# Kernel tuning notes

Hardware: AMD Instinct MI355X
Metric: run time of the kernel (lower is better)

The kernel has to match this reference:

```python
import jax, jax.numpy as jnp
import numpy as np

N, E = 20000, 320000
D_IN, HID, HEADS, OUT = 256, 64, 8, 64
K1 = int(np.ceil(0.75 * N))   # 15000 nodes after pool1
K2 = int(np.ceil(0.75 * K1))  # 11250 nodes after pool2
NEG = -1e30


def setup_inputs():
    key = jax.random.key(0)
    ks = jax.random.split(key, 24)
    s = 0.1
    rn = lambda k, shape: jax.random.normal(k, shape, jnp.float32) * s
    HH = HEADS * HID  # 512
    p = {}
    p["x"] = jax.random.normal(ks[0], (N, D_IN), jnp.float32)
    p["edge_index"] = jax.random.randint(ks[1], (2, E), 0, N, dtype=jnp.int32)
    # gat1: GATv2Conv(D_IN -> HID, heads=HEADS), concat output dim HH
    p["g1_wl"] = rn(ks[2], (D_IN, HH)); p["g1_wr"] = rn(ks[3], (D_IN, HH))
    p["g1_att"] = rn(ks[4], (HEADS, HID)); p["g1_b"] = jnp.zeros((HH,), jnp.float32)
    # pool1 scoring GNN: GATConv(HH -> 1, heads=1) + SelectTopK weight
    p["p1_w"] = rn(ks[5], (HH, 1)); p["p1_asrc"] = rn(ks[6], (1,)); p["p1_adst"] = rn(ks[7], (1,))
    p["p1_b"] = jnp.zeros((1,), jnp.float32); p["p1_sel"] = rn(ks[8], (1,)) + 0.5
    # gat2: GATv2Conv(HH -> HID, heads=1)
    p["g2_wl"] = rn(ks[9], (HH, HID)); p["g2_wr"] = rn(ks[10], (HH, HID))
    p["g2_att"] = rn(ks[11], (1, HID)); p["g2_b"] = jnp.zeros((HID,), jnp.float32)
    # pool2 scoring GNN: GATConv(HID -> 1)
    p["p2_w"] = rn(ks[12], (HID, 1)); p["p2_asrc"] = rn(ks[13], (1,)); p["p2_adst"] = rn(ks[14], (1,))
    p["p2_b"] = jnp.zeros((1,), jnp.float32); p["p2_sel"] = rn(ks[15], (1,)) + 0.5
    # MLP head
    p["l1_w"] = rn(ks[16], (2 * HH, HH)); p["l1_b"] = jnp.zeros((HH,), jnp.float32)
    d2 = OUT * (HEADS // 2); d3 = OUT * (HEADS // 4)
    p["l2_w"] = rn(ks[17], (HH, d2)); p["l2_b"] = jnp.zeros((d2,), jnp.float32)
    p["l3_w"] = rn(ks[18], (d2, d3)); p["l3_b"] = jnp.zeros((d3,), jnp.float32)
    p["l4_w"] = rn(ks[19], (d3, 2)); p["l4_b"] = jnp.zeros((2,), jnp.float32)
    return p


def _seg_softmax(e, dst, valid, n):
    # numerically stable segment softmax over destination nodes; invalid edges -> 0
    e = jnp.where(valid[:, None], e, NEG)
    m = jax.ops.segment_max(e, dst, num_segments=n)
    ex = jnp.exp(e - m[dst])
    ex = jnp.where(valid[:, None], ex, 0.0)
    den = jax.ops.segment_sum(ex, dst, num_segments=n)
    return ex / den[dst]


def gatv2(x, src, dst, valid, wl, wr, att, b):
    # GATv2Conv: score = att . LeakyReLU(Wl x_src + Wr x_dst), segment softmax, concat heads
    n = x.shape[0]
    h, c = att.shape
    xl = (x @ wl).reshape(n, h, c)
    xr = (x @ wr).reshape(n, h, c)
    loop = jnp.arange(n, dtype=src.dtype)  # add_self_loops=True
    s = jnp.concatenate([src, loop]); d = jnp.concatenate([dst, loop])
    v = jnp.concatenate([valid, jnp.ones((n,), bool)])
    m = jax.nn.leaky_relu(xl[s] + xr[d], 0.2)          # [E', H, C]
    e = jnp.einsum("ehc,hc->eh", m, att)               # [E', H]
    a = _seg_softmax(e, d, v, n)
    out = jax.ops.segment_sum(a[..., None] * xl[s], d, num_segments=n)
    return out.reshape(n, h * c) + b


def gat_score(x, src, dst, valid, w, asrc, adst, b):
    # GATConv(in -> 1, heads=1): per-node scalar projection score
    n = x.shape[0]
    xl = x @ w                                          # [n, 1]
    al = (xl * asrc).sum(-1); ar = (xl * adst).sum(-1)  # [n]
    loop = jnp.arange(n, dtype=src.dtype)
    s = jnp.concatenate([src, loop]); d = jnp.concatenate([dst, loop])
    v = jnp.concatenate([valid, jnp.ones((n,), bool)])
    e = jax.nn.leaky_relu(al[s] + ar[d], 0.2)[:, None]
    a = _seg_softmax(e, d, v, n)
    return jax.ops.segment_sum(a * xl[s], d, num_segments=n) + b


def sag_pool(x, src, dst, valid, k, w, asrc, adst, b, sel_w):
    # SAGPooling: GNN score -> tanh -> top-k -> x[perm]*score, edge filtering via mask
    attn = gat_score(x, src, dst, valid, w, asrc, adst, b)           # [n, 1]
    score = jnp.tanh((attn * sel_w).sum(-1) / jnp.linalg.norm(sel_w))  # SelectTopK
    vals, perm = jax.lax.top_k(score, k)
    xp = x[perm] * vals[:, None]
    new_id = jnp.full((x.shape[0],), -1, src.dtype).at[perm].set(jnp.arange(k, dtype=src.dtype))
    s2, d2 = new_id[src], new_id[dst]
    v2 = valid & (s2 >= 0) & (d2 >= 0)
    return xp, jnp.where(v2, s2, 0), jnp.where(v2, d2, 0), v2


def _forward(x, edge_index, g1_wl, g1_wr, g1_att, g1_b, p1_w, p1_asrc, p1_adst, p1_b, p1_sel,
             g2_wl, g2_wr, g2_att, g2_b, p2_w, p2_asrc, p2_adst, p2_b, p2_sel,
             l1_w, l1_b, l2_w, l2_b, l3_w, l3_b, l4_w, l4_b):
    src, dst = edge_index[0], edge_index[1]
    valid = jnp.ones((src.shape[0],), bool)
    h = jax.nn.relu(gatv2(x, src, dst, valid, g1_wl, g1_wr, g1_att, g1_b))
    h, s1, d1, v1 = sag_pool(h, src, dst, valid, K1, p1_w, p1_asrc, p1_adst, p1_b, p1_sel)
    # single graph -> global pools are plain reductions over nodes
    x1 = jnp.concatenate([h.max(0, keepdims=True), h.mean(0, keepdims=True)], axis=1)
    h2 = jax.nn.relu(gatv2(h, s1, d1, v1, g2_wl, g2_wr, g2_att, g2_b))
    h2, _, _, _ = sag_pool(h2, s1, d1, v1, K2, p2_w, p2_asrc, p2_adst, p2_b, p2_sel)
    gmax = jnp.tile(h2.max(0, keepdims=True), (1, HEADS))
    gmean = jnp.tile(h2.mean(0, keepdims=True), (1, HEADS))
    z = x1 + jnp.concatenate([gmax, gmean], axis=1)
    z = jax.nn.relu(z @ l1_w + l1_b)   # dropout is identity at eval
    z = jax.nn.relu(z @ l2_w + l2_b)
    z = jax.nn.relu(z @ l3_w + l3_b)
    logits = z @ l4_w + l4_b
    return logits, jax.nn.softmax(logits, axis=-1)


def reference(x, edge_index, g1_wl, g1_wr, g1_att, g1_b, p1_w, p1_asrc, p1_adst, p1_b, p1_sel,
              g2_wl, g2_wr, g2_att, g2_b, p2_w, p2_asrc, p2_adst, p2_b, p2_sel,
              l1_w, l1_b, l2_w, l2_b, l3_w, l3_b, l4_w, l4_b):
    return _forward(x, edge_index, g1_wl, g1_wr, g1_att, g1_b, p1_w, p1_asrc, p1_adst, p1_b, p1_sel,
                    g2_wl, g2_wr, g2_att, g2_b, p2_w, p2_asrc, p2_adst, p2_b, p2_sel,
                    l1_w, l1_b, l2_w, l2_b, l3_w, l3_b, l4_w, l4_b)
```

## Files before the change

### kernel.cpp

```cpp
#include <hip/hip_runtime.h>
#include <math.h>

#define N_NODES 20000
#define E_EDGES 320000
#define DIN     256
#define HHD     512
#define HIDD    64
#define NHEADS  8
#define K1N     15000
#define K2N     11250

typedef unsigned short u16;
typedef __attribute__((ext_vector_type(8))) short bf16x8;
typedef __attribute__((ext_vector_type(4))) float f32x4;

static inline int cdiv(long long a, long long b) { return (int)((a + b - 1) / b); }

__device__ __forceinline__ void atomicMaxF(float* addr, float val) {
  int* ai = (int*)addr;
  int old = __float_as_int(*addr);
  while (__int_as_float(old) < val) {
    int assumed = old;
    old = atomicCAS(ai, assumed, __float_as_int(val));
    if (old == assumed) break;
  }
}

__device__ __forceinline__ u16 f2bf(float x) {
  unsigned u = __float_as_uint(x);
  return (u16)((u + 0x7FFFu + ((u >> 16) & 1u)) >> 16);
}
__device__ __forceinline__ float bfval(u16 b) { return __uint_as_float(((unsigned)b) << 16); }

__device__ __forceinline__ void unpk8(uint4 u, float* v) {
  v[0] = __uint_as_float(u.x << 16); v[1] = __uint_as_float(u.x & 0xffff0000u);
  v[2] = __uint_as_float(u.y << 16); v[3] = __uint_as_float(u.y & 0xffff0000u);
  v[4] = __uint_as_float(u.z << 16); v[5] = __uint_as_float(u.z & 0xffff0000u);
  v[6] = __uint_as_float(u.w << 16); v[7] = __uint_as_float(u.w & 0xffff0000u);
}

__device__ __forceinline__ unsigned fkey(float s) {
  unsigned b = __float_as_uint(s);
  return (b & 0x80000000u) ? ~b : (b | 0x80000000u);
}

__global__ void init_all(int* deg1, float* pools) {
  int i = blockIdx.x * blockDim.x + threadIdx.x;
  if (i < N_NODES) deg1[i] = 0;
  else {
    int idx = i - N_NODES;
    if (idx < 1152)
      pools[idx] = (idx < 512 || (idx >= 1024 && idx < 1088)) ? -INFINITY : 0.f;
  }
}

__global__ void conv_fused(const float* __restrict__ A, const int* __restrict__ perm,
                           const float* __restrict__ scalev,
                           u16* __restrict__ ah, u16* __restrict__ al, int M, int K,
                           const float* __restrict__ w1, const float* __restrict__ w2,
                           u16* __restrict__ wh, u16* __restrict__ wl, int ncHalf,
                           int aBlocks) {
  if ((int)blockIdx.x < aBlocks) {
    long long i = (long long)blockIdx.x * blockDim.x + threadIdx.x;
    long long e0 = i * 4;
    if (e0 >= (long long)M * K) return;
    int row = (int)(e0 / K), col = (int)(e0 % K);
    int ar = perm ? perm[row] : row;
    float4 v = *(const float4*)(A + (size_t)ar * K + col);
    if (scalev) { float s = scalev[ar]; v.x *= s; v.y *= s; v.z *= s; v.w *= s; }
    u16 h0 = f2bf(v.x), h1 = f2bf(v.y), h2 = f2bf(v.z), h3 = f2bf(v.w);
    u16 l0 = f2bf(v.x - bfval(h0)), l1 = f2bf(v.y - bfval(h1));
    u16 l2 = f2bf(v.z - bfval(h2)), l3 = f2bf(v.w - bfval(h3));
    uint2 hp, lp;
    hp.x = (unsigned)h0 | ((unsigned)h1 << 16); hp.y = (unsigned)h2 | ((unsigned)h3 << 16);
    lp.x = (unsigned)l0 | ((unsigned)l1 << 16); lp.y = (unsigned)l2 | ((unsigned)l3 << 16);
    *(uint2*)(ah + e0) = hp;
    *(uint2*)(al + e0) = lp;
  } else {
    int i = (blockIdx.x - aBlocks) * blockDim.x + threadIdx.x;
    int NT = 2 * ncHalf;
    if (i >= NT * K) return;
    int n = i % NT, k = i / NT;
    float v = (n < ncHalf) ? w1[(size_t)k * ncHalf + n] : w2[(size_t)k * ncHalf + (n - ncHalf)];
    u16 h = f2bf(v);
    u16 l = f2bf(v - bfval(h));
    wh[(size_t)n * K + k] = h;
    wl[(size_t)n * K + k] = l;
  }
}

template<int BT, bool OUTBF, int NPROD>
__global__ __launch_bounds__(256) void gemm_bf16x3(const u16* __restrict__ ah,
                                                   const u16* __restrict__ al,
                                                   const u16* __restrict__ wh,
                                                   const u16* __restrict__ wl,
                                                   void* __restrict__ c1v,
                                                   void* __restrict__ c2v,
                                                   int M, int K, int ncHalf) {
  constexpr int F = BT / 32;
  __shared__ u16 Ah[BT][42], Al[BT][42], Bh[BT][42];
  __shared__ u16 Bl[NPROD == 3 ? BT : 1][NPROD == 3 ? 42 : 1];
  int tid = threadIdx.x;
  int lane = tid & 63, wid = tid >> 6;
  int wr = (wid >> 1) * (BT / 2), wc = (wid & 1) * (BT / 2);
  int brow = blockIdx.y * BT, bcol = blockIdx.x * BT;
  int fr = lane & 15, kg = lane >> 4;
  f32x4 acc[F][F];
#pragma unroll
  for (int i = 0; i < F; i++)
#pragma unroll
    for (int j = 0; j < F; j++) acc[i][j] = (f32x4){0.f, 0.f, 0.f, 0.f};

  for (int k0 = 0; k0 < K; k0 += 32) {
    constexpr int ITER = (BT * 32) / (256 * 8);
#pragma unroll
    for (int i = 0; i < ITER; i++) {
      int pos = tid + i * 256;
      int row = pos >> 2;
      int kc = (pos & 3) * 8;
      int gr = brow + row;
      float4 z = make_float4(0.f, 0.f, 0.f, 0.f);
      float4 vah = (gr < M) ? *(const float4*)(ah + (size_t)gr * K + k0 + kc) : z;
      float4 val = (gr < M) ? *(const float4*)(al + (size_t)gr * K + k0 + kc) : z;
      *(float4*)(&Ah[row][kc]) = vah;
      *(float4*)(&Al[row][kc]) = val;
      int gn = bcol + row;
      *(float4*)(&Bh[row][kc]) = *(const float4*)(wh + (size_t)gn * K + k0 + kc);
      if (NPROD == 3)
        *(float4*)(&Bl[row][kc]) = *(const float4*)(wl + (size_t)gn * K + k0 + kc);
    }
    __syncthreads();
    bf16x8 fa_h[F], fa_l[F], fb_h[F], fb_l[F];
#pragma unroll
    for (int t = 0; t < F; t++) {
      fa_h[t] = *(const bf16x8*)(&Ah[wr + t * 16 + fr][kg * 8]);
      fa_l[t] = *(const bf16x8*)(&Al[wr + t * 16 + fr][kg * 8]);
      fb_h[t] = *(const bf16x8*)(&Bh[wc + t * 16 + fr][kg * 8]);
      if (NPROD == 3)
        fb_l[t] = *(const bf16x8*)(&Bl[wc + t * 16 + fr][kg * 8]);
    }
#pragma unroll
    for (int i = 0; i < F; i++)
#pragma unroll
      for (int j = 0; j < F; j++) {
        acc[i][j] = __builtin_amdgcn_mfma_f32_16x16x32_bf16(fa_h[i], fb_h[j], acc[i][j], 0, 0, 0);
        acc[i][j] = __builtin_amdgcn_mfma_f32_16x16x32_bf16(fa_l[i], fb_h[j], acc[i][j], 0, 0, 0);
        if (NPROD == 3)
          acc[i][j] = __builtin_amdgcn_mfma_f32_16x16x32_bf16(fa_h[i], fb_l[j], acc[i][j], 0, 0, 0);
      }
    __syncthreads();
  }
#pragma unroll
  for (int i = 0; i < F; i++) {
    int r0 = brow + wr + i * 16 + kg * 4;
#pragma unroll
    for (int j = 0; j < F; j++) {
      int cg = bcol + wc + j * 16 + fr;
      bool first = (cg < ncHalf);
      int cc = first ? cg : cg - ncHalf;
#pragma unroll
      for (int r = 0; r < 4; r++) {
        int gr = r0 + r;
        if (gr < M) {
          if (OUTBF) {
            u16* cp = first ? (u16*)c1v : (u16*)c2v;
            cp[(size_t)gr * ncHalf + cc] = f2bf(acc[i][j][r]);
          } else {
            float* cp = first ? (float*)c1v : (float*)c2v;
            cp[(size_t)gr * ncHalf + cc] = acc[i][j][r];
          }
        }
      }
    }
  }
}

__global__ void deg_count(const int* __restrict__ src, const int* __restrict__ dst,
                          const int* __restrict__ newid, int* __restrict__ deg,
                          int nloops) {
  int i = blockIdx.x * blockDim.x + threadIdx.x;
  if (i >= E_EDGES + nloops) return;
  int d;
  if (i < E_EDGES) {
    if (newid) {
      int s = newid[src[i]]; d = newid[dst[i]];
      if (s < 0 || d < 0) return;
    } else d = dst[i];
  } else d = i - E_EDGES;
  atomicAdd(&deg[d], 1);
}

__global__ __launch_bounds__(1024) void scan_excl(const int* deg, int* rowptr,
                                                  int* cursor, int n) {
  __shared__ int wsum[16];
  __shared__ int carry;
  int tid = threadIdx.x, lane = tid & 63, wid = tid >> 6;
  if (tid == 0) { carry = 0; rowptr[0] = 0; }
  __syncthreads();
  for (int base = 0; base < n; base += 1024) {
    int v = (base + tid < n) ? deg[base + tid] : 0;
    int s = v;
#pragma unroll
    for (int off = 1; off < 64; off <<= 1) {
      int t = __shfl_up(s, off);
      if (lane >= off) s += t;
    }
    if (lane == 63) wsum[wid] = s;
    __syncthreads();
    if (wid == 0) {
      int w = (lane < 16) ? wsum[lane] : 0;
#pragma unroll
      for (int off = 1; off < 16; off <<= 1) {
        int t = __shfl_up(w, off);
        if (lane >= off) w += t;
      }
      if (lane < 16) wsum[lane] = w;
    }
    __syncthreads();
    int incl = s + (wid > 0 ? wsum[wid - 1] : 0) + carry;
    if (base + tid < n) { rowptr[base + tid + 1] = incl; cursor[base + tid] = incl - v; }
    __syncthreads();
    if (tid == 1023) carry = incl;
    __syncthreads();
  }
}

__global__ void csr_scatter(const int* __restrict__ src, const int* __restrict__ dst,
                            const int* __restrict__ newid, int* __restrict__ cursor,
                            int* __restrict__ csr_s, int nloops) {
  int i = blockIdx.x * blockDim.x + threadIdx.x;
  if (i >= E_EDGES + nloops) return;
  int s, d;
  if (i < E_EDGES) {
    s = src[i]; d = dst[i];
    if (newid) {
      s = newid[s]; d = newid[d];
      if (s < 0 || d < 0) return;
    }
  } else s = d = i - E_EDGES;
  int pos = atomicAdd(&cursor[d], 1);
  csr_s[pos] = s;
}

__global__ __launch_bounds__(256) void gat1_fused(const int* __restrict__ rowptr,
                                                  const int* __restrict__ csr_s,
                                                  const u16* __restrict__ xlb,
                                                  const u16* __restrict__ xrb,
                                                  const float* __restrict__ att,
                                                  const float* __restrict__ bias,
                                                  const float* __restrict__ pw,
                                                  float* __restrict__ out,
                                                  float* __restrict__ xls) {
  int lane = threadIdx.x & 63;
  long long t = (long long)blockIdx.x * blockDim.x + threadIdx.x;
  int d = (int)(t >> 6);
  if (d >= N_NODES) return;
  int base = lane * 8;
  float4 a0 = *(const float4*)(att + base);
  float4 a1 = *(const float4*)(att + base + 4);
  float r[8];
  unpk8(*(const uint4*)(xrb + (size_t)d * HHD + base), r);
  float m = -INFINITY, den = 0.f;
  float acc[8] = {0.f, 0.f, 0.f, 0.f, 0.f, 0.f, 0.f, 0.f};
  int b0 = rowptr[d];
  int cnt = rowptr[d + 1] - b0;
  const int* sp = csr_s + b0;

  auto online = [&](uint4 u) {
    float v[8];
    unpk8(u, v);
    float p, tv;
    tv = v[0] + r[0]; tv = tv > 0.f ? tv : 0.2f * tv; p  = tv * a0.x;
    tv = v[1] + r[1]; tv = tv > 0.f ? tv : 0.2f * tv; p += tv * a0.y;
    tv = v[2] + r[2]; tv = tv > 0.f ? tv : 0.2f * tv; p += tv * a0.z;
    tv = v[3] + r[3]; tv = tv > 0.f ? tv : 0.2f * tv; p += tv * a0.w;
    tv = v[4] + r[4]; tv = tv > 0.f ? tv : 0.2f * tv; p += tv * a1.x;
    tv = v[5] + r[5]; tv = tv > 0.f ? tv : 0.2f * tv; p += tv * a1.y;
    tv = v[6] + r[6]; tv = tv > 0.f ? tv : 0.2f * tv; p += tv * a1.z;
    tv = v[7] + r[7]; tv = tv > 0.f ? tv : 0.2f * tv; p += tv * a1.w;
    p += __shfl_xor(p, 1); p += __shfl_xor(p, 2); p += __shfl_xor(p, 4);
    float nm = fmaxf(m, p);
    float w  = __expf(p - nm);
    float sc = __expf(m - nm);
    den = den * sc + w;
#pragma unroll
    for (int k = 0; k < 8; k++) acc[k] = acc[k] * sc + w * v[k];
    m = nm;
  };

  uint4 zz = make_uint4(0u, 0u, 0u, 0u);
  uint4 A = *(const uint4*)(xlb + (size_t)sp[0] * HHD + base);
  uint4 B = (cnt > 1) ? *(const uint4*)(xlb + (size_t)sp[1] * HHD + base) : zz;
  uint4 C = (cnt > 2) ? *(const uint4*)(xlb + (size_t)sp[2] * HHD + base) : zz;
  uint4 D = (cnt > 3) ? *(const uint4*)(xlb + (size_t)sp[3] * HHD + base) : zz;
  int j = 0;
  for (; j + 4 <= cnt; j += 4) {
    uint4 u = A;
    if (j + 4 < cnt) A = *(const uint4*)(xlb + (size_t)sp[j + 4] * HHD + base);
    online(u);
    u = B;
    if (j + 5 < cnt) B = *(const uint4*)(xlb + (size_t)sp[j + 5] * HHD + base);
    online(u);
    u = C;
    if (j + 6 < cnt) C = *(const uint4*)(xlb + (size_t)sp[j + 6] * HHD + base);
    online(u);
    u = D;
    if (j + 7 < cnt) D = *(const uint4*)(xlb + (size_t)sp[j + 7] * HHD + base);
    online(u);
  }
  if (j < cnt) {
    online(A);
    if (j + 1 < cnt) {
      online(B);
      if (j + 2 < cnt) online(C);
    }
  }

  float inv = 1.f / den;
  float4 b0v = *(const float4*)(bias + base);
  float4 b1v = *(const float4*)(bias + base + 4);
  float o[8];
  o[0] = acc[0] * inv + b0v.x; o[1] = acc[1] * inv + b0v.y;
  o[2] = acc[2] * inv + b0v.z; o[3] = acc[3] * inv + b0v.w;
  o[4] = acc[4] * inv + b1v.x; o[5] = acc[5] * inv + b1v.y;
  o[6] = acc[6] * inv + b1v.z; o[7] = acc[7] * inv + b1v.w;
#pragma unroll
  for (int k = 0; k < 8; k++) o[k] = o[k] > 0.f ? o[k] : 0.f;
  float* op = out + (size_t)d * HHD + base;
  *(float4*)(op)     = make_float4(o[0], o[1], o[2], o[3]);
  *(float4*)(op + 4) = make_float4(o[4], o[5], o[6], o[7]);
  float4 w0 = *(const float4*)(pw + base);
  float4 w1 = *(const float4*)(pw + base + 4);
  float sdot = o[0]*w0.x + o[1]*w0.y + o[2]*w0.z + o[3]*w0.w
             + o[4]*w1.x + o[5]*w1.y + o[6]*w1.z + o[7]*w1.w;
#pragma unroll
  for (int off = 32; off > 0; off >>= 1) sdot += __shfl_xor(sdot, off);
  if (lane == 0) xls[d] = sdot;
}

__global__ __launch_bounds__(256) void gat2_fused(const int* __restrict__ rowptr,
                                                  const int* __restrict__ csr_s,
                                                  const float* __restrict__ xl,
                                                  const float* __restrict__ xr,
                                                  const float* __restrict__ att,
                                                  const float* __restrict__ bias,
                                                  const float* __restrict__ pw,
                                                  float* __restrict__ out,
                                                  float* __restrict__ xls, int n) {
  int lane = threadIdx.x & 63;
  int grp = lane >> 4, li = lane & 15;
  long long t = (long long)blockIdx.x * blockDim.x + threadIdx.x;
  int wv = (int)(t >> 6);
  int d = wv * 4 + grp;
  if (d >= n) return;
  int c0 = li * 4;
  float4 av = *(const float4*)(att + c0);
  float4 rv = *(const float4*)(xr + (size_t)d * HIDD + c0);
  float m = -INFINITY, den = 0.f;
  float4 acc = make_float4(0.f, 0.f, 0.f, 0.f);
  int b0 = rowptr[d];
  int cnt = rowptr[d + 1] - b0;
  const int* sp = csr_s + b0;

  auto online = [&](float4 v) {
    float p, tv;
    tv = v.x + rv.x; tv = tv > 0.f ? tv : 0.2f * tv; p  = tv * av.x;
    tv = v.y + rv.y; tv = tv > 0.f ? tv : 0.2f * tv; p += tv * av.y;
    tv = v.z + rv.z; tv = tv > 0.f ? tv : 0.2f * tv; p += tv * av.z;
    tv = v.w + rv.w; tv = tv > 0.f ? tv : 0.2f * tv; p += tv * av.w;
    p += __shfl_xor(p, 1); p += __shfl_xor(p, 2); p += __shfl_xor(p, 4); p += __shfl_xor(p, 8);
    float nm = fmaxf(m, p);
    float w  = __expf(p - nm);
    float sc = __expf(m - nm);
    den = den * sc + w;
    acc.x = acc.x * sc + w * v.x;
    acc.y = acc.y * sc + w * v.y;
    acc.z = acc.z * sc + w * v.z;
    acc.w = acc.w * sc + w * v.w;
    m = nm;
  };

  float4 zz = make_float4(0.f, 0.f, 0.f, 0.f);
  float4 A = *(const float4*)(xl + (size_t)sp[0] * HIDD + c0);
  float4 B = (cnt > 1) ? *(const float4*)(xl + (size_t)sp[1] * HIDD + c0) : zz;
  int j = 0;
  for (; j + 2 <= cnt; j += 2) {
    float4 v = A;
    if (j + 2 < cnt) A = *(const float4*)(xl + (size_t)sp[j + 2] * HIDD + c0);
    online(v);
    v = B;
    if (j + 3 < cnt) B = *(const float4*)(xl + (size_t)sp[j + 3] * HIDD + c0);
    online(v);
  }
  if (j < cnt) online(A);

  float inv = 1.f / den;
  float4 bv = *(const float4*)(bias + c0);
  float4 o;
  o.x = acc.x * inv + bv.x; o.y = acc.y * inv + bv.y;
  o.z = acc.z * inv + bv.z; o.w = acc.w * inv + bv.w;
  o.x = o.x > 0.f ? o.x : 0.f; o.y = o.y > 0.f ? o.y : 0.f;
  o.z = o.z > 0.f ? o.z : 0.f; o.w = o.w > 0.f ? o.w : 0.f;
  *(float4*)(out + (size_t)d * HIDD + c0) = o;
  float4 wv4 = *(const float4*)(pw + c0);
  float sdot = o.x * wv4.x + o.y * wv4.y + o.z * wv4.z + o.w * wv4.w;
  sdot += __shfl_xor(sdot, 1); sdot += __shfl_xor(sdot, 2);
  sdot += __shfl_xor(sdot, 4); sdot += __shfl_xor(sdot, 8);
  if (li == 0) xls[d] = sdot;
}

__global__ __launch_bounds__(256) void pool_score(const int* __restrict__ rowptr,
                                                  const int* __restrict__ csr_s,
                                                  const float* __restrict__ xls,
                                                  const float* __restrict__ asrc,
                                                  const float* __restrict__ adst,
                                                  const float* __restrict__ bias,
                                                  const float* __restrict__ sel,
                                                  float* __restrict__ score, int n) {
  int d = blockIdx.x * blockDim.x + threadIdx.x;
  if (d >= n) return;
  float as = asrc[0], ad = adst[0];
  float ar = xls[d] * ad;
  int b0 = rowptr[d];
  int cnt = rowptr[d + 1] - b0;
  const int* sp = csr_s + b0;
  float m = -INFINITY, den = 0.f, num = 0.f;
  auto upd = [&](float xs) {
    float e = xs * as + ar;
    e = e > 0.f ? e : 0.2f * e;
    float nm = fmaxf(m, e);
    float scv = __expf(m - nm);
    float ex = __expf(e - nm);
    den = den * scv + ex;
    num = num * scv + ex * xs;
    m = nm;
  };
  float xA = xls[sp[0]];
  float xB = (cnt > 1) ? xls[sp[1]] : 0.f;
  float xC = (cnt > 2) ? xls[sp[2]] : 0.f;
  float xD = (cnt > 3) ? xls[sp[3]] : 0.f;
  int j = 0;
  for (; j + 4 <= cnt; j += 4) {
    float x1 = xA;
    if (j + 4 < cnt) xA = xls[sp[j + 4]];
    upd(x1);
    float x2 = xB;
    if (j + 5 < cnt) xB = xls[sp[j + 5]];
    upd(x2);
    float x3 = xC;
    if (j + 6 < cnt) xC = xls[sp[j + 6]];
    upd(x3);
    float x4 = xD;
    if (j + 7 < cnt) xD = xls[sp[j + 7]];
    upd(x4);
  }
  if (j < cnt) {
    upd(xA);
    if (j + 1 < cnt) {
      upd(xB);
      if (j + 2 < cnt) upd(xC);
    }
  }
  float attn = num / den + bias[0];
  float sv = sel[0];
  score[d] = tanhf(attn * sv / fabsf(sv));
}

__global__ __launch_bounds__(1024) void tk_topk(const float* __restrict__ score, int n, int k,
                                                int* __restrict__ newid, int* __restrict__ perm,
                                                int* __restrict__ zbuf, int zn) {
  __shared__ unsigned bins[2048];
  __shared__ unsigned wsum[16];
  __shared__ unsigned sb[4];
  int tid = threadIdx.x, lane = tid & 63, wid = tid >> 6;

  for (int i = tid; i < zn; i += 1024) zbuf[i] = 0;

  unsigned pref = 0;
  unsigned kneed = (unsigned)k;

  for (int level = 0; level < 3; level++) {
    const int shift = (level == 0) ? 21 : (level == 1) ? 10 : 0;
    const unsigned mask = (level == 2) ? 1023u : 2047u;
    for (int b = tid; b < 2048; b += 1024) bins[b] = 0;
    __syncthreads();
    for (int i = tid; i < n; i += 1024) {
      unsigned key = fkey(score[i]);
      bool match = (level == 0) ? true
                 : (level == 1) ? ((key >> 21) == pref)
                                : ((key >> 10) == pref);
      if (match) atomicAdd(&bins[(key >> shift) & mask], 1u);
    }
    __syncthreads();
    unsigned c0 = bins[2 * tid], c1 = bins[2 * tid + 1];
    unsigned v = c0 + c1;
    unsigned s = v;
#pragma unroll
    for (int off = 1; off < 64; off <<= 1) {
      unsigned t2 = __shfl_up(s, off);
      if (lane >= off) s += t2;
    }
    if (lane == 63) wsum[wid] = s;
    __syncthreads();
    if (wid == 0) {
      unsigned w = (lane < 16) ? wsum[lane] : 0;
#pragma unroll
      for (int off = 1; off < 16; off <<= 1) {
        unsigned t2 = __shfl_up(w, off);
        if (lane >= off) w += t2;
      }
      if (lane < 16) wsum[lane] = w;
    }
    __syncthreads();
    unsigned incl = s + (wid > 0 ? wsum[wid - 1] : 0);
    unsigned excl = incl - v;
    if (tid == 1023) sb[0] = incl;
    __syncthreads();
    unsigned TOT = sb[0];
    unsigned target = TOT - kneed;
    unsigned ip0 = excl + c0;
    unsigned ip1 = ip0 + c1;
    if (excl <= target && target < ip0) { sb[1] = 2u * tid;     sb[2] = TOT - ip0; }
    if (ip0  <= target && target < ip1) { sb[1] = 2u * tid + 1; sb[2] = TOT - ip1; }
    __syncthreads();
    pref = (pref << ((level == 2) ? 10 : 11)) | sb[1];
    kneed -= sb[2];
    __syncthreads();
  }
  const unsigned U = pref, rem = kneed;

  unsigned carry = 0;
  for (int base = 0; base < n; base += 1024) {
    int i = base + tid;
    bool valid = i < n;
    unsigned key = valid ? fkey(score[i]) : 0u;
    unsigned gt  = (valid && key >  U) ? 1u : 0u;
    unsigned tie = (valid && key == U) ? 1u : 0u;
    unsigned v = gt | (tie << 16);
    unsigned s = v;
#pragma unroll
    for (int off = 1; off < 64; off <<= 1) {
      unsigned t2 = __shfl_up(s, off);
      if (lane >= off) s += t2;
    }
    if (lane == 63) wsum[wid] = s;
    __syncthreads();
    if (wid == 0) {
      unsigned w = (lane < 16) ? wsum[lane] : 0;
#pragma unroll
      for (int off = 1; off < 16; off <<= 1) {
        unsigned t2 = __shfl_up(w, off);
        if (lane >= off) w += t2;
      }
      if (lane < 16) wsum[lane] = w;
    }
    __syncthreads();
    unsigned incl = s + (wid > 0 ? wsum[wid - 1] : 0);
    unsigned pfx = (incl - v) + carry;
    unsigned gtpfx = pfx & 0xFFFFu, tiepfx = pfx >> 16;
    unsigned tsel = (tiepfx < rem) ? tiepfx : rem;
    bool selq = gt || (tie && tiepfx < rem);
    unsigned id = gtpfx + tsel;
    if (valid) {
      newid[i] = selq ? (int)id : -1;
      if (selq) perm[id] = i;
    }
    if (tid == 1023) sb[0] = incl + carry;
    __syncthreads();
    carry = sb[0];
    __syncthreads();
  }
}

__global__ __launch_bounds__(256) void col_pool_conv(const float* __restrict__ X,
                                                     const int* __restrict__ perm,
                                                     const float* __restrict__ scalev,
                                                     float* __restrict__ omax,
                                                     float* __restrict__ osum,
                                                     u16* __restrict__ ah, u16* __restrict__ al,
                                                     const float* __restrict__ w1,
                                                     const float* __restrict__ w2,
                                                     u16* __restrict__ wh, u16* __restrict__ wl,
                                                     int cpBlocks) {
  int tid = threadIdx.x;
  if ((int)blockIdx.x < cpBlocks) {
    float mx[2] = {-INFINITY, -INFINITY};
    float sm[2] = {0.f, 0.f};
    int rpb = (K1N + cpBlocks - 1) / cpBlocks;
    int rbeg = blockIdx.x * rpb;
    int rend = min(K1N, rbeg + rpb);
    for (int r = rbeg; r < rend; r++) {
      int orow = perm[r];
      float sc = scalev[orow];
      const float* row = X + (size_t)orow * HHD;
#pragma unroll
      for (int sg = 0; sg < 2; sg++) {
        int c = sg * 256 + tid;
        float v = row[c] * sc;
        mx[sg] = fmaxf(mx[sg], v);
        sm[sg] += v;
        u16 h = f2bf(v);
        u16 l = f2bf(v - bfval(h));
        ah[(size_t)r * HHD + c] = h;
        al[(size_t)r * HHD + c] = l;
      }
    }
    if (rbeg < rend) {
#pragma unroll
      for (int sg = 0; sg < 2; sg++) {
        int c = sg * 256 + tid;
        atomicMaxF(&omax[c], mx[sg]);
        atomicAdd(&osum[c], sm[sg]);
      }
    }
  } else {
    int i = (blockIdx.x - cpBlocks) * 256 + tid;
    const int NT = 2 * HIDD;
    if (i >= NT * HHD) return;
    int n = i % NT, k = i / NT;
    float v = (n < HIDD) ? w1[(size_t)k * HIDD + n] : w2[(size_t)k * HIDD + (n - HIDD)];
    u16 h = f2bf(v);
    u16 l = f2bf(v - bfval(h));
    wh[(size_t)n * HHD + k] = h;
    wl[(size_t)n * HHD + k] = l;
  }
}

__global__ __launch_bounds__(256) void col_pool(const float* __restrict__ X,
                                                const int* __restrict__ perm,
                                                const float* __restrict__ scalev,
                                                int rows, int C,
                                                float* __restrict__ omax, float* __restrict__ osum) {
  int tid = threadIdx.x;
  float mx = -INFINITY, sm = 0.f;
  int rpb = (rows + gridDim.x - 1) / gridDim.x;
  int rbeg = blockIdx.x * rpb;
  int rend = min(rows, rbeg + rpb);
  for (int r = rbeg; r < rend; r++) {
    int orow = perm[r];
    float sc = scalev[orow];
    int c = tid;
    if (c < C) {
      float v = X[(size_t)orow * C + c] * sc;
      mx = fmaxf(mx, v);
      sm += v;
    }
  }
  if (rbeg < rend && tid < C) {
    atomicMaxF(&omax[tid], mx);
    atomicAdd(&osum[tid], sm);
  }
}

__global__ __launch_bounds__(256) void mlp_l1(const float* __restrict__ pools,
                                              const float* __restrict__ w1,
                                              const float* __restrict__ b1,
                                              float* __restrict__ z1out) {
  __shared__ float z[1024];
  __shared__ float red[16][17];
  int t = threadIdx.x;
  for (int i = t; i < 1024; i += 256) {
    float xv = (i < 512) ? pools[i] : pools[i] * (1.f / K1N);
    float gv = (i < 512) ? pools[1024 + (i & 63)] : pools[1088 + (i & 63)] * (1.f / K2N);
    z[i] = xv + gv;
  }
  __syncthreads();
  int jl = t & 15, ch = t >> 4;
  int j = blockIdx.x * 16 + jl;
  float p = 0.f;
  for (int k = ch * 64; k < ch * 64 + 64; k++) p += z[k] * w1[(size_t)k * 512 + j];
  red[ch][jl] = p;
  __syncthreads();
  if (t < 16) {
    float s = b1[blockIdx.x * 16 + t];
    for (int c = 0; c < 16; c++) s += red[c][t];
    z1out[blockIdx.x * 16 + t] = s > 0.f ? s : 0.f;
  }
}

template<int NIN>
__global__ __launch_bounds__(256) void mlp_layer(const float* __restrict__ in,
                                                 const float* __restrict__ w,
                                                 const float* __restrict__ b,
                                                 float* __restrict__ out, int nout) {
  __shared__ float red[16][17];
  int t = threadIdx.x;
  int jl = t & 15, ch = t >> 4;
  int j = blockIdx.x * 16 + jl;
  constexpr int CH = NIN / 16;
  float p = 0.f;
  for (int k = ch * CH; k < (ch + 1) * CH; k++) p += in[k] * w[(size_t)k * nout + j];
  red[ch][jl] = p;
  __syncthreads();
  if (t < 16) {
    float s = b[blockIdx.x * 16 + t];
    for (int c = 0; c < 16; c++) s += red[c][t];
    out[blockIdx.x * 16 + t] = s > 0.f ? s : 0.f;
  }
}

__global__ __launch_bounds__(128) void mlp_final(const float* __restrict__ z3,
                                                 const float* __restrict__ w4,
                                                 const float* __restrict__ b4,
                                                 float* __restrict__ out) {
  int t = threadIdx.x;
  float v = z3[t];
  float p0 = v * w4[2 * t], p1 = v * w4[2 * t + 1];
#pragma unroll
  for (int off = 32; off > 0; off >>= 1) {
    p0 += __shfl_xor(p0, off);
    p1 += __shfl_xor(p1, off);
  }
  __shared__ float s0[2], s1[2];
  if ((t & 63) == 0) { s0[t >> 6] = p0; s1[t >> 6] = p1; }
  __syncthreads();
  if (t == 0) {
    float l0 = s0[0] + s0[1] + b4[0], l1 = s1[0] + s1[1] + b4[1];
    float m = fmaxf(l0, l1);
    float e0 = __expf(l0 - m), e1 = __expf(l1 - m);
    float s = e0 + e1;
    out[0] = l0; out[1] = l1;
    out[2] = e0 / s; out[3] = e1 / s;
  }
}

extern "C" void kernel_launch(void* const* d_in, const int* in_sizes, int n_in,
                              void* d_out, int out_size, void* d_ws, size_t ws_size,
                              hipStream_t stream) {
  const float* x       = (const float*)d_in[0];
  const int*   ei      = (const int*)d_in[1];
  const float* g1_wl   = (const float*)d_in[2];
  const float* g1_wr   = (const float*)d_in[3];
  const float* g1_att  = (const float*)d_in[4];
  const float* g1_b    = (const float*)d_in[5];
  const float* p1_w    = (const float*)d_in[6];
  const float* p1_asrc = (const float*)d_in[7];
  const float* p1_adst = (const float*)d_in[8];
  const float* p1_b    = (const float*)d_in[9];
  const float* p1_sel  = (const float*)d_in[10];
  const float* g2_wl   = (const float*)d_in[11];
  const float* g2_wr   = (const float*)d_in[12];
  const float* g2_att  = (const float*)d_in[13];
  const float* g2_b    = (const float*)d_in[14];
  const float* p2_w    = (const float*)d_in[15];
  const float* p2_asrc = (const float*)d_in[16];
  const float* p2_adst = (const float*)d_in[17];
  const float* p2_b    = (const float*)d_in[18];
  const float* p2_sel  = (const float*)d_in[19];
  const float* l1_w    = (const float*)d_in[20];
  const float* l1_b    = (const float*)d_in[21];
  const float* l2_w    = (const float*)d_in[22];
  const float* l2_b    = (const float*)d_in[23];
  const float* l3_w    = (const float*)d_in[24];
  const float* l3_b    = (const float*)d_in[25];
  const float* l4_w    = (const float*)d_in[26];
  const float* l4_b    = (const float*)d_in[27];

  const int* src = ei;
  const int* dst = ei + E_EDGES;

  if (ws_size < (size_t)33440000 * 4) return;
  float* ws  = (float*)d_ws;
  float* xl1 = ws;
  float* xr1 = ws + 10240000;
  float* h1  = ws + 20480000;
  float* aux = ws + 30720000;

  int*   csr_s1   = (int*)aux;
  int*   rowptr1  = (int*)(aux + 340000);
  int*   deg1     = (int*)(aux + 360064);
  int*   newid1   = (int*)(aux + 400064);
  float* xls1     = aux + 420064;
  float* scr1     = aux + 440064;
  float* pools    = aux + 460064;
  float* x1max    = pools;
  float* x1sum    = pools + 512;
  float* g2max    = pools + 1024;
  float* g2sum    = pools + 1088;
  int*   perm1    = (int*)(aux + 461248);
  float* z1       = aux + 481248;
  float* z2       = aux + 481760;
  float* z3       = aux + 482016;

  u16* xl1b = (u16*)xl1;
  u16* xr1b = (u16*)xr1;

  u16* ah1 = (u16*)h1;
  u16* al1 = ah1 + 5120000;
  u16* wh1 = al1 + 5120000;
  u16* wl1 = wh1 + 262144;

  u16* ah2 = (u16*)xl1;
  u16* al2 = ah2 + 7680000;
  u16* wh2 = al2 + 7680000;
  u16* wl2 = wh2 + 65536;

  float* a2 = xr1;
  float* xl2      = a2;
  float* xr2      = a2 + 960000;
  float* h2       = a2 + 1920000;
  int*   csr_s2   = (int*)(a2 + 2880000);
  int*   rowptr2  = (int*)(a2 + 3215000);
  int*   deg2     = (int*)(a2 + 3230016);
  int*   newid2   = (int*)(a2 + 3260016);
  float* xls2     = a2 + 3275016;
  float* scr2     = a2 + 3290016;
  int*   perm2    = (int*)(a2 + 3305016);

  dim3 b256(256);
  const int E1 = E_EDGES + N_NODES;
  const int E2 = E_EDGES + K1N;

  init_all<<<cdiv(N_NODES + 1152, 256), b256, 0, stream>>>(deg1, pools);
  deg_count<<<cdiv(E1, 256), b256, 0, stream>>>(src, dst, nullptr, deg1, N_NODES);
  scan_excl<<<1, 1024, 0, stream>>>(deg1, rowptr1, deg1, N_NODES);
  csr_scatter<<<cdiv(E1, 256), b256, 0, stream>>>(src, dst, nullptr, deg1, csr_s1, N_NODES);

  {
    int aBlocks = cdiv((long long)N_NODES * DIN / 4, 256);
    int wBlocks = cdiv(2 * HHD * DIN, 256);
    conv_fused<<<aBlocks + wBlocks, b256, 0, stream>>>(
        x, nullptr, nullptr, ah1, al1, N_NODES, DIN, g1_wl, g1_wr, wh1, wl1, HHD, aBlocks);
  }
  gemm_bf16x3<128, true, 2><<<dim3(2 * HHD / 128, cdiv(N_NODES, 128)), b256, 0, stream>>>(
      ah1, al1, wh1, wl1, xl1b, xr1b, N_NODES, DIN, HHD);
  gat1_fused<<<cdiv((long long)N_NODES * 64, 256), b256, 0, stream>>>(
      rowptr1, csr_s1, xl1b, xr1b, g1_att, g1_b, p1_w, h1, xls1);

  pool_score<<<cdiv(N_NODES, 256), b256, 0, stream>>>(rowptr1, csr_s1, xls1,
                                                      p1_asrc, p1_adst, p1_b, p1_sel, scr1, N_NODES);
  tk_topk<<<1, 1024, 0, stream>>>(scr1, N_NODES, K1N, newid1, perm1, deg2, 15000);
  {
    int cpBlocks = 256;
    int wBlocks = cdiv(2 * HIDD * HHD, 256);
    col_pool_conv<<<cpBlocks + wBlocks, b256, 0, stream>>>(
        h1, perm1, scr1, x1max, x1sum, ah2, al2, g2_wl, g2_wr, wh2, wl2, cpBlocks);
  }

  deg_count<<<cdiv(E2, 256), b256, 0, stream>>>(src, dst, newid1, deg2, K1N);
  scan_excl<<<1, 1024, 0, stream>>>(deg2, rowptr2, deg2, K1N);
  csr_scatter<<<cdiv(E2, 256), b256, 0, stream>>>(src, dst, newid1, deg2, csr_s2, K1N);

  gemm_bf16x3<64, false, 3><<<dim3(2 * HIDD / 64, cdiv(K1N, 64)), b256, 0, stream>>>(
      ah2, al2, wh2, wl2, xl2, xr2, K1N, HHD, HIDD);
  gat2_fused<<<cdiv((long long)K1N * 16, 256), b256, 0, stream>>>(
      rowptr2, csr_s2, xl2, xr2, g2_att, g2_b, p2_w, h2, xls2, K1N);

  pool_score<<<cdiv(K1N, 256), b256, 0, stream>>>(rowptr2, csr_s2, xls2,
                                                  p2_asrc, p2_adst, p2_b, p2_sel, scr2, K1N);
  tk_topk<<<1, 1024, 0, stream>>>(scr2, K1N, K2N, newid2, perm2, nullptr, 0);
  col_pool<<<128, b256, 0, stream>>>(h2, perm2, scr2, K2N, HIDD, g2max, g2sum);

  mlp_l1<<<32, b256, 0, stream>>>(pools, l1_w, l1_b, z1);
  mlp_layer<512><<<16, b256, 0, stream>>>(z1, l2_w, l2_b, z2, 256);
  mlp_layer<256><<<8, b256, 0, stream>>>(z2, l3_w, l3_b, z3, 128);
  mlp_final<<<1, 128, 0, stream>>>(z3, l4_w, l4_b, (float*)d_out);
}
```

Before: 478.1 us.

## Fuse degree counting into conversion kernels and serialize-chunk scans

Folds the degree-count pass into the existing conversion kernels as extra blocks, which removes two launches. The exclusive scan and the top-k index assignment switch from a looped block scan with many barriers to per-thread sequential chunks plus one block scan. The online softmax in both GAT aggregation kernels now branches, so a new maximum costs one exp instead of two. In exchange, the per-thread chunk reads are strided and uncoalesced, and the branches may diverge.

```diff
diff --git a/kernel.cpp b/kernel.cpp
--- a/kernel.cpp
+++ b/kernel.cpp
@@ -59,7 +59,8 @@
                            u16* __restrict__ ah, u16* __restrict__ al, int M, int K,
                            const float* __restrict__ w1, const float* __restrict__ w2,
                            u16* __restrict__ wh, u16* __restrict__ wl, int ncHalf,
-                           int aBlocks) {
+                           int aBlocks, int wBlocks,
+                           const int* __restrict__ dc_dst, int* __restrict__ dc_deg, int dc_n) {
   if ((int)blockIdx.x < aBlocks) {
     long long i = (long long)blockIdx.x * blockDim.x + threadIdx.x;
     long long e0 = i * 4;
@@ -76,7 +77,7 @@
     lp.x = (unsigned)l0 | ((unsigned)l1 << 16); lp.y = (unsigned)l2 | ((unsigned)l3 << 16);
     *(uint2*)(ah + e0) = hp;
     *(uint2*)(al + e0) = lp;
-  } else {
+  } else if ((int)blockIdx.x < aBlocks + wBlocks) {
     int i = (blockIdx.x - aBlocks) * blockDim.x + threadIdx.x;
     int NT = 2 * ncHalf;
     if (i >= NT * K) return;
@@ -86,6 +87,11 @@
     u16 l = f2bf(v - bfval(h));
     wh[(size_t)n * K + k] = h;
     wl[(size_t)n * K + k] = l;
+  } else {
+    int i = (blockIdx.x - aBlocks - wBlocks) * blockDim.x + threadIdx.x;
+    if (i >= E_EDGES + dc_n) return;
+    int d = (i < E_EDGES) ? dc_dst[i] : i - E_EDGES;
+    atomicAdd(&dc_deg[d], 1);
   }
 }
 
@@ -175,54 +181,41 @@
   }
 }
 
-__global__ void deg_count(const int* __restrict__ src, const int* __restrict__ dst,
-                          const int* __restrict__ newid, int* __restrict__ deg,
-                          int nloops) {
-  int i = blockIdx.x * blockDim.x + threadIdx.x;
-  if (i >= E_EDGES + nloops) return;
-  int d;
-  if (i < E_EDGES) {
-    if (newid) {
-      int s = newid[src[i]]; d = newid[dst[i]];
-      if (s < 0 || d < 0) return;
-    } else d = dst[i];
-  } else d = i - E_EDGES;
-  atomicAdd(&deg[d], 1);
-}
-
 __global__ __launch_bounds__(1024) void scan_excl(const int* deg, int* rowptr,
                                                   int* cursor, int n) {
   __shared__ int wsum[16];
-  __shared__ int carry;
   int tid = threadIdx.x, lane = tid & 63, wid = tid >> 6;
-  if (tid == 0) { carry = 0; rowptr[0] = 0; }
+  int C = (n + 1023) >> 10;
+  int beg = tid * C, end = min(n, beg + C);
+  int s = 0;
+  for (int i = beg; i < end; i++) s += deg[i];
+  int ws = s;
+#pragma unroll
+  for (int off = 1; off < 64; off <<= 1) {
+    int t = __shfl_up(ws, off);
+    if (lane >= off) ws += t;
+  }
+  if (lane == 63) wsum[wid] = ws;
   __syncthreads();
-  for (int base = 0; base < n; base += 1024) {
-    int v = (base + tid < n) ? deg[base + tid] : 0;
-    int s = v;
-#pragma unroll
-    for (int off = 1; off < 64; off <<= 1) {
-      int t = __shfl_up(s, off);
-      if (lane >= off) s += t;
-    }
-    if (lane == 63) wsum[wid] = s;
-    __syncthreads();
-    if (wid == 0) {
-      int w = (lane < 16) ? wsum[lane] : 0;
-#pragma unroll
-      for (int off = 1; off < 16; off <<= 1) {
-        int t = __shfl_up(w, off);
-        if (lane >= off) w += t;
-      }
-      if (lane < 16) wsum[lane] = w;
-    }
-    __syncthreads();
-    int incl = s + (wid > 0 ? wsum[wid - 1] : 0) + carry;
-    if (base + tid < n) { rowptr[base + tid + 1] = incl; cursor[base + tid] = incl - v; }
-    __syncthreads();
-    if (tid == 1023) carry = incl;
-    __syncthreads();
-  }
+  if (wid == 0) {
+    int w = (lane < 16) ? wsum[lane] : 0;
+#pragma unroll
+    for (int off = 1; off < 16; off <<= 1) {
+      int t = __shfl_up(w, off);
+      if (lane >= off) w += t;
+    }
+    if (lane < 16) wsum[lane] = w;
+  }
+  __syncthreads();
+  int incl = ws + (wid > 0 ? wsum[wid - 1] : 0);
+  int run = incl - s;
+  for (int i = beg; i < end; i++) {
+    int d = deg[i];
+    cursor[i] = run;
+    rowptr[i + 1] = run + d;
+    run += d;
+  }
+  if (tid == 0) rowptr[0] = 0;
 }
 
 __global__ void csr_scatter(const int* __restrict__ src, const int* __restrict__ dst,
@@ -279,13 +272,18 @@
     tv = v[6] + r[6]; tv = tv > 0.f ? tv : 0.2f * tv; p += tv * a1.z;
     tv = v[7] + r[7]; tv = tv > 0.f ? tv : 0.2f * tv; p += tv * a1.w;
     p += __shfl_xor(p, 1); p += __shfl_xor(p, 2); p += __shfl_xor(p, 4);
-    float nm = fmaxf(m, p);
-    float w  = __expf(p - nm);
-    float sc = __expf(m - nm);
-    den = den * sc + w;
-#pragma unroll
-    for (int k = 0; k < 8; k++) acc[k] = acc[k] * sc + w * v[k];
-    m = nm;
+    if (p > m) {
+      float sc = __expf(m - p);
+      den = den * sc + 1.f;
+#pragma unroll
+      for (int k = 0; k < 8; k++) acc[k] = acc[k] * sc + v[k];
+      m = p;
+    } else {
+      float w = __expf(p - m);
+      den += w;
+#pragma unroll
+      for (int k = 0; k < 8; k++) acc[k] += w * v[k];
+    }
   };
 
   uint4 zz = make_uint4(0u, 0u, 0u, 0u);
@@ -369,15 +367,22 @@
     tv = v.z + rv.z; tv = tv > 0.f ? tv : 0.2f * tv; p += tv * av.z;
     tv = v.w + rv.w; tv = tv > 0.f ? tv : 0.2f * tv; p += tv * av.w;
     p += __shfl_xor(p, 1); p += __shfl_xor(p, 2); p += __shfl_xor(p, 4); p += __shfl_xor(p, 8);
-    float nm = fmaxf(m, p);
-    float w  = __expf(p - nm);
-    float sc = __expf(m - nm);
-    den = den * sc + w;
-    acc.x = acc.x * sc + w * v.x;
-    acc.y = acc.y * sc + w * v.y;
-    acc.z = acc.z * sc + w * v.z;
-    acc.w = acc.w * sc + w * v.w;
-    m = nm;
+    if (p > m) {
+      float sc = __expf(m - p);
+      den = den * sc + 1.f;
+      acc.x = acc.x * sc + v.x;
+      acc.y = acc.y * sc + v.y;
+      acc.z = acc.z * sc + v.z;
+      acc.w = acc.w * sc + v.w;
+      m = p;
+    } else {
+      float w = __expf(p - m);
+      den += w;
+      acc.x += w * v.x;
+      acc.y += w * v.y;
+      acc.z += w * v.z;
+      acc.w += w * v.w;
+    }
   };
 
   float4 zz = make_float4(0.f, 0.f, 0.f, 0.f);
@@ -529,46 +534,51 @@
   }
   const unsigned U = pref, rem = kneed;
 
-  unsigned carry = 0;
-  for (int base = 0; base < n; base += 1024) {
-    int i = base + tid;
-    bool valid = i < n;
-    unsigned key = valid ? fkey(score[i]) : 0u;
-    unsigned gt  = (valid && key >  U) ? 1u : 0u;
-    unsigned tie = (valid && key == U) ? 1u : 0u;
-    unsigned v = gt | (tie << 16);
-    unsigned s = v;
-#pragma unroll
-    for (int off = 1; off < 64; off <<= 1) {
-      unsigned t2 = __shfl_up(s, off);
-      if (lane >= off) s += t2;
-    }
-    if (lane == 63) wsum[wid] = s;
-    __syncthreads();
-    if (wid == 0) {
-      unsigned w = (lane < 16) ? wsum[lane] : 0;
-#pragma unroll
-      for (int off = 1; off < 16; off <<= 1) {
-        unsigned t2 = __shfl_up(w, off);
-        if (lane >= off) w += t2;
-      }
-      if (lane < 16) wsum[lane] = w;
-    }
-    __syncthreads();
-    unsigned incl = s + (wid > 0 ? wsum[wid - 1] : 0);
-    unsigned pfx = (incl - v) + carry;
-    unsigned gtpfx = pfx & 0xFFFFu, tiepfx = pfx >> 16;
-    unsigned tsel = (tiepfx < rem) ? tiepfx : rem;
-    bool selq = gt || (tie && tiepfx < rem);
-    unsigned id = gtpfx + tsel;
-    if (valid) {
-      newid[i] = selq ? (int)id : -1;
-      if (selq) perm[id] = i;
-    }
-    if (tid == 1023) sb[0] = incl + carry;
-    __syncthreads();
-    carry = sb[0];
-    __syncthreads();
+  int C = (n + 1023) >> 10;
+  int beg = tid * C, end = min(n, beg + C);
+  unsigned gt = 0, tie = 0;
+  for (int i = beg; i < end; i++) {
+    unsigned key = fkey(score[i]);
+    gt  += (key >  U);
+    tie += (key == U);
+  }
+  unsigned v = gt | (tie << 16);
+  unsigned s = v;
+#pragma unroll
+  for (int off = 1; off < 64; off <<= 1) {
+    unsigned t2 = __shfl_up(s, off);
+    if (lane >= off) s += t2;
+  }
+  if (lane == 63) wsum[wid] = s;
+  __syncthreads();
+  if (wid == 0) {
+    unsigned w = (lane < 16) ? wsum[lane] : 0;
+#pragma unroll
+    for (int off = 1; off < 16; off <<= 1) {
+      unsigned t2 = __shfl_up(w, off);
+      if (lane >= off) w += t2;
+    }
+    if (lane < 16) wsum[lane] = w;
+  }
+  __syncthreads();
+  unsigned incl = s + (wid > 0 ? wsum[wid - 1] : 0);
+  unsigned pfx = incl - v;
+  unsigned run_gt = pfx & 0xFFFFu, run_tie = pfx >> 16;
+  for (int i = beg; i < end; i++) {
+    unsigned key = fkey(score[i]);
+    if (key > U) {
+      unsigned id = run_gt + (run_tie < rem ? run_tie : rem);
+      newid[i] = (int)id;
+      perm[id] = i;
+      run_gt++;
+    } else if (key == U) {
+      if (run_tie < rem) {
+        unsigned id = run_gt + run_tie;
+        newid[i] = (int)id;
+        perm[id] = i;
+      } else newid[i] = -1;
+      run_tie++;
+    } else newid[i] = -1;
   }
 }
 
@@ -581,7 +591,11 @@
                                                      const float* __restrict__ w1,
                                                      const float* __restrict__ w2,
                                                      u16* __restrict__ wh, u16* __restrict__ wl,
-                                                     int cpBlocks) {
+                                                     int cpBlocks, int wBlocks,
+                                                     const int* __restrict__ src,
+                                                     const int* __restrict__ dst,
+                                                     const int* __restrict__ newid,
+                                                     int* __restrict__ deg2) {
   int tid = threadIdx.x;
   if ((int)blockIdx.x < cpBlocks) {
     float mx[2] = {-INFINITY, -INFINITY};
@@ -613,7 +627,7 @@
         atomicAdd(&osum[c], sm[sg]);
       }
     }
-  } else {
+  } else if ((int)blockIdx.x < cpBlocks + wBlocks) {
     int i = (blockIdx.x - cpBlocks) * 256 + tid;
     const int NT = 2 * HIDD;
     if (i >= NT * HHD) return;
@@ -623,6 +637,15 @@
     u16 l = f2bf(v - bfval(h));
     wh[(size_t)n * HHD + k] = h;
     wl[(size_t)n * HHD + k] = l;
+  } else {
+    int i = (blockIdx.x - cpBlocks - wBlocks) * 256 + tid;
+    if (i >= E_EDGES + K1N) return;
+    int d;
+    if (i < E_EDGES) {
+      int s = newid[src[i]]; d = newid[dst[i]];
+      if (s < 0 || d < 0) return;
+    } else d = i - E_EDGES;
+    atomicAdd(&deg2[d], 1);
   }
 }
 
@@ -812,16 +835,17 @@
   const int E2 = E_EDGES + K1N;
 
   init_all<<<cdiv(N_NODES + 1152, 256), b256, 0, stream>>>(deg1, pools);
-  deg_count<<<cdiv(E1, 256), b256, 0, stream>>>(src, dst, nullptr, deg1, N_NODES);
-  scan_excl<<<1, 1024, 0, stream>>>(deg1, rowptr1, deg1, N_NODES);
-  csr_scatter<<<cdiv(E1, 256), b256, 0, stream>>>(src, dst, nullptr, deg1, csr_s1, N_NODES);
-
   {
     int aBlocks = cdiv((long long)N_NODES * DIN / 4, 256);
     int wBlocks = cdiv(2 * HHD * DIN, 256);
-    conv_fused<<<aBlocks + wBlocks, b256, 0, stream>>>(
-        x, nullptr, nullptr, ah1, al1, N_NODES, DIN, g1_wl, g1_wr, wh1, wl1, HHD, aBlocks);
-  }
+    int dBlocks = cdiv(E1, 256);
+    conv_fused<<<aBlocks + wBlocks + dBlocks, b256, 0, stream>>>(
+        x, nullptr, nullptr, ah1, al1, N_NODES, DIN, g1_wl, g1_wr, wh1, wl1, HHD,
+        aBlocks, wBlocks, dst, deg1, N_NODES);
+  }
+  scan_excl<<<1, 1024, 0, stream>>>(deg1, rowptr1, deg1, N_NODES);
+  csr_scatter<<<cdiv(E1, 256), b256, 0, stream>>>(src, dst, nullptr, deg1, csr_s1, N_NODES);
+
   gemm_bf16x3<128, true, 2><<<dim3(2 * HHD / 128, cdiv(N_NODES, 128)), b256, 0, stream>>>(
       ah1, al1, wh1, wl1, xl1b, xr1b, N_NODES, DIN, HHD);
   gat1_fused<<<cdiv((long long)N_NODES * 64, 256), b256, 0, stream>>>(
@@ -833,11 +857,12 @@
   {
     int cpBlocks = 256;
     int wBlocks = cdiv(2 * HIDD * HHD, 256);
-    col_pool_conv<<<cpBlocks + wBlocks, b256, 0, stream>>>(
-        h1, perm1, scr1, x1max, x1sum, ah2, al2, g2_wl, g2_wr, wh2, wl2, cpBlocks);
-  }
-
-  deg_count<<<cdiv(E2, 256), b256, 0, stream>>>(src, dst, newid1, deg2, K1N);
+    int dBlocks = cdiv(E2, 256);
+    col_pool_conv<<<cpBlocks + wBlocks + dBlocks, b256, 0, stream>>>(
+        h1, perm1, scr1, x1max, x1sum, ah2, al2, g2_wl, g2_wr, wh2, wl2,
+        cpBlocks, wBlocks, src, dst, newid1, deg2);
+  }
+
   scan_excl<<<1, 1024, 0, stream>>>(deg2, rowptr2, deg2, K1N);
   csr_scatter<<<cdiv(E2, 256), b256, 0, stream>>>(src, dst, newid1, deg2, csr_s2, K1N);
 
```

Result: slower. 491.8 us (+2.9%).
